# Kernel optimization log

Hardware: AMD Instinct MI355X
Metric: run time of the kernel (lower is better)

The kernel has to match this reference:

```python
import jax, jax.numpy as jnp
import numpy as np

NPRE = 8        # diffusion iterations (production default 8000; math identical per step)
DEPS = 0.1
LAMBDA = 0.24
K_PM = 0.03     # exp(log(0.03)) buffer in the 'none' branch
ALPHA = 0.7
SIGMA_FREQ = 0.1


def _g_pm(x, K):
    # Perona-Malik conductance g(x) = 1 / (1 + |x^2| / K^2)
    return 1.0 / (1.0 + jnp.abs(x * x) / (K * K))


def _gaussian_blur3(x, sigma):
    # Replicates torch create_gaussian_kernel(3, sigma): linspace(-3//2, 3//2, 3) = [-2, -0.5, 1]
    xs = jnp.linspace(-2.0, 1.0, 3)
    g1 = jnp.exp(-(xs ** 2) / (2.0 * sigma * sigma))
    g1 = g1 / g1.sum()
    k2 = jnp.outer(g1, g1).astype(x.dtype)            # [3,3]
    C = x.shape[1]
    k = jnp.broadcast_to(k2, (C, 1, 3, 3))
    xp = jnp.pad(x, ((0, 0), (0, 0), (1, 1), (1, 1)), mode='reflect')
    return jax.lax.conv_general_dilated(
        xp, k, window_strides=(1, 1), padding='VALID',
        dimension_numbers=('NCHW', 'OIHW', 'NCHW'), feature_group_count=C)


def _edge_coeffs(I, K):
    # c(I): FFT high-pass edge response + finite differences -> Perona-Malik coefficients
    b, c_, h, w = I.shape
    F = jnp.fft.fft2(I, norm='ortho')
    y = jnp.linspace(-1.0, 1.0, h)[:, None]
    xg = jnp.linspace(-1.0, 1.0, w)[None, :]
    hf_mask = (jnp.sqrt(xg * xg + y * y) > 0.5).astype(I.dtype)   # [h,w]
    er = jnp.real(jnp.fft.ifft2(F * hf_mask, norm='ortho'))
    dv = jnp.abs(I[:, :, 1:, :] - I[:, :, :-1, :]) + er[:, :, 1:, :]
    dh = jnp.abs(I[:, :, :, 1:] - I[:, :, :, :-1]) + er[:, :, :, 1:]
    cv = _g_pm(jnp.mean(dv, axis=1, keepdims=True), K)   # [b,1,h-1,w]
    ch = _g_pm(jnp.mean(dh, axis=1, keepdims=True), K)   # [b,1,h,w-1]
    return cv, ch


def _diffuse_step(cv, ch, I, l=LAMBDA):
    # frequency-domain smoothing branch
    Ff = jnp.fft.fft2(I, norm='ortho')
    sr = _gaussian_blur3(jnp.real(Ff), SIGMA_FREQ)
    si = _gaussian_blur3(jnp.imag(Ff), SIGMA_FREQ)
    I_freq = jnp.real(jnp.fft.ifft2(jax.lax.complex(sr, si), norm='ortho'))
    dv = I[:, :, 1:, :] - I[:, :, :-1, :]
    dh = I[:, :, :, 1:] - I[:, :, :, :-1]
    I = ALPHA * I + (1.0 - ALPHA) * I_freq
    tv = l * cv * dv
    th = l * ch * dh
    I = I.at[:, :, 1:, :].add(-tv).at[:, :, :-1, :].add(tv)
    I = I.at[:, :, :, 1:].add(-th).at[:, :, :, :-1].add(th)
    return I


def _adjust_step(img, source, mask_inv, eps=1e-8):
    b, c_, h, w = img.shape
    sh, sw = source.shape[2], source.shape[3]
    fh, fw = h // sh, w // sw
    # AdaptiveAvgPool2d((sh,sw)) with integer factor == block mean
    img_ss = img.reshape(b, c_, sh, fh, sw, fw).mean(axis=(3, 5))
    ratio_ss = jnp.where(mask_inv, jnp.ones_like(img_ss), source / (img_ss + eps))
    # nearest upsample with integer factor == repeat
    ratio = jnp.repeat(jnp.repeat(ratio_ss, fh, axis=2), fw, axis=3)
    return img * ratio


def setup_inputs() -> dict:
    key = jax.random.key(0)
    k1, k2, k3, k4 = jax.random.split(key, 4)
    guide = jax.random.normal(k1, (4, 3, 1024, 1024), dtype=jnp.float32)
    source = jax.random.uniform(k2, (4, 1, 128, 128), dtype=jnp.float32)
    mask_lr = jax.random.uniform(k3, (4, 1, 128, 128), dtype=jnp.float32)
    y_bicubic = jax.random.uniform(k4, (4, 1, 1024, 1024), dtype=jnp.float32)
    return {"guide": guide, "source": source, "mask_lr": mask_lr, "y_bicubic": y_bicubic}


def reference(guide, source, mask_lr, y_bicubic):
    # depth shift when source.min() <= deps (uniform[0,1) source -> effectively always)
    shift = jnp.where(jnp.min(source) <= DEPS, DEPS, 0.0).astype(source.dtype)
    source = source + shift
    img = y_bicubic + shift
    mask_inv = mask_lr < 0.5

    # 'none' feature extractor: guide_feats = cat([guide, img], 1) -> [B,4,H,W]
    feats = jnp.concatenate([guide, img], axis=1)
    cv, ch = _edge_coeffs(feats, K_PM)

    def step(I, _):
        I = _diffuse_step(cv, ch, I)
        I = _adjust_step(I, source, mask_inv)
        return I, None

    img, _ = jax.lax.scan(step, img, None, length=NPRE)
    return img - shift
```

## Files before the change

kernel.cpp:

```cpp
#include <hip/hip_runtime.h>
#include <hip/hip_fp16.h>

namespace {

constexpr int H = 1024, W = 1024, NB = 4;
constexpr int SH = 128, SW = 128;
constexpr float LAM = 0.24f;
constexpr float KK = 0.03f * 0.03f;
constexpr float DEPS_V = 0.1f;
constexpr float FFT_SCALE = 1.0f / (1024.0f * 1024.0f);
constexpr int COL_LO = 256, NCOL = 512;

__device__ __forceinline__ float2 cadd(float2 a, float2 b) { return make_float2(a.x + b.x, a.y + b.y); }
__device__ __forceinline__ float2 csub(float2 a, float2 b) { return make_float2(a.x - b.x, a.y - b.y); }
__device__ __forceinline__ float2 cmul(float2 a, float2 b) {
  return make_float2(a.x * b.x - a.y * b.y, a.x * b.y + a.y * b.x);
}
__device__ __forceinline__ int phys2(int e) { return e + (e >> 4); }

__global__ void k_shift_part(const float* __restrict__ src, float* __restrict__ partial) {
  int t = threadIdx.x;
  int b0 = blockIdx.x * 1024;
  float m = fminf(fminf(src[b0 + t], src[b0 + t + 256]),
                  fminf(src[b0 + t + 512], src[b0 + t + 768]));
  for (int o = 32; o > 0; o >>= 1) m = fminf(m, __shfl_xor(m, o));
  __shared__ float sm[4];
  if ((t & 63) == 0) sm[t >> 6] = m;
  __syncthreads();
  if (t == 0) partial[blockIdx.x] = fminf(fminf(sm[0], sm[1]), fminf(sm[2], sm[3]));
}

__global__ void k_shift_fin(const float* __restrict__ partial, float* __restrict__ shiftp) {
  int t = threadIdx.x;
  float m = partial[t];
  for (int o = 32; o > 0; o >>= 1) m = fminf(m, __shfl_xor(m, o));
  if (t == 0) shiftp[0] = (m <= DEPS_V) ? DEPS_V : 0.0f;
}

template <int NS, bool INV>
__device__ __forceinline__ void r4_butterfly(float2 v[4], int j, float2 r[4]) {
  if (NS > 1) {
    int p = j & (NS - 1);
    float sn, cs;
    sincospif((INV ? 1.0f : -1.0f) * (float)p * (1.0f / (float)(2 * NS)), &sn, &cs);
    float2 w1 = make_float2(cs, sn);
    float2 w2 = cmul(w1, w1);
    float2 w3 = cmul(w2, w1);
    v[1] = cmul(v[1], w1);
    v[2] = cmul(v[2], w2);
    v[3] = cmul(v[3], w3);
  }
  float2 a0 = cadd(v[0], v[2]), a2 = csub(v[0], v[2]);
  float2 a1 = cadd(v[1], v[3]), a3 = csub(v[1], v[3]);
  a3 = INV ? make_float2(-a3.y, a3.x) : make_float2(a3.y, -a3.x);
  r[0] = cadd(a0, a1);
  r[2] = csub(a0, a1);
  r[1] = cadd(a2, a3);
  r[3] = csub(a2, a3);
}

template <int NS, bool INV>
__device__ __forceinline__ void r4_stage_lds(float2 v[4], float2* dst, int j) {
  float2 r[4];
  r4_butterfly<NS, INV>(v, j, r);
  int p = j & (NS - 1);
  int base = ((j - p) << 2) + p;
#pragma unroll
  for (int k = 0; k < 4; ++k) dst[phys2(base + k * NS)] = r[k];
}

__device__ __forceinline__ void lds_load4(const float2* src, float2 v[4], int j) {
#pragma unroll
  for (int k = 0; k < 4; ++k) v[k] = src[phys2(j + k * 256)];
}

template <bool INV>
__device__ void fft1024(float2 v[4], float2* b0, float2* b1, int j) {
  r4_stage_lds<1, INV>(v, b0, j);
  __syncthreads();
  lds_load4(b0, v, j);
  r4_stage_lds<4, INV>(v, b1, j);
  __syncthreads();
  lds_load4(b1, v, j);
  r4_stage_lds<16, INV>(v, b0, j);
  __syncthreads();
  lds_load4(b0, v, j);
  r4_stage_lds<64, INV>(v, b1, j);
  __syncthreads();
  lds_load4(b1, v, j);
  float2 r[4];
  r4_butterfly<256, INV>(v, j, r);
#pragma unroll
  for (int k = 0; k < 4; ++k) v[k] = r[k];
}

__global__ void k_rowfft_fwd(const float* __restrict__ guide, const float* __restrict__ ybic,
                             const float* __restrict__ shiftp, float2* __restrict__ A) {
  __shared__ float2 b0[1088], b1[1088];
  int b = blockIdx.y, y0 = blockIdx.x * 2, j = threadIdx.x;
  float sh = shiftp[0];
  const float* g0 = guide + ((size_t)(b * 3 + 0) * H + y0) * W;
  const float* g1 = guide + ((size_t)(b * 3 + 1) * H + y0) * W;
  const float* g2 = guide + ((size_t)(b * 3 + 2) * H + y0) * W;
  const float* yb = ybic + ((size_t)b * H + y0) * W;
  float2 v[4];
#pragma unroll
  for (int k = 0; k < 4; ++k) {
    int x = j + k * 256;
    float s0 = g0[x] + g1[x] + g2[x] + (yb[x] + sh);
    float s1 = g0[x + W] + g1[x + W] + g2[x + W] + (yb[x + W] + sh);
    v[k] = make_float2(s0, s1);
  }
  fft1024<false>(v, b0, b1, j);
#pragma unroll
  for (int k = 0; k < 4; ++k) b0[phys2(j + k * 256)] = v[k];
  __syncthreads();
  float2* o0 = A + ((size_t)b * H + y0) * W;
  float2* o1 = o0 + W;
#pragma unroll
  for (int k = 0; k < 4; ++k) {
    int m = j + k * 256;
    float2 Zm = v[k];
    float2 Zc = b0[phys2((1024 - m) & 1023)];
    o0[m] = make_float2(0.5f * (Zm.x + Zc.x), 0.5f * (Zm.y - Zc.y));
    o1[m] = make_float2(0.5f * (Zm.y + Zc.y), 0.5f * (Zc.x - Zm.x));
  }
}

__global__ void k_transpose_fwd(const float2* __restrict__ A, float2* __restrict__ Bc) {
  __shared__ float2 tile[32][33];
  int b = blockIdx.z;
  int c0 = blockIdx.x * 32, y0 = blockIdx.y * 32;
  const float2* ip = A + (size_t)b * H * W;
  float2* op = Bc + (size_t)b * NCOL * H;
#pragma unroll
  for (int k = 0; k < 4; ++k)
    tile[threadIdx.y + k * 8][threadIdx.x] =
        ip[(size_t)(y0 + threadIdx.y + k * 8) * W + (COL_LO + c0 + threadIdx.x)];
  __syncthreads();
#pragma unroll
  for (int k = 0; k < 4; ++k)
    op[(size_t)(c0 + threadIdx.y + k * 8) * H + (y0 + threadIdx.x)] =
        tile[threadIdx.x][threadIdx.y + k * 8];
}

__global__ void k_colfft_mask(float2* __restrict__ Bc) {
  __shared__ float2 b0[1088], b1[1088];
  int b = blockIdx.y, r = blockIdx.x, j = threadIdx.x;
  int k2 = COL_LO + r;
  double xj = -1.0 + 2.0 * (double)k2 / 1023.0;
  double xj2 = xj * xj;
  float2* row = Bc + ((size_t)b * NCOL + r) * H;
  float2 v[4];
#pragma unroll
  for (int k = 0; k < 4; ++k) v[k] = row[j + k * 256];
  fft1024<false>(v, b0, b1, j);
#pragma unroll
  for (int k = 0; k < 4; ++k) {
    int i = j + k * 256;
    double yv = -1.0 + 2.0 * (double)i / 1023.0;
    if (xj2 + yv * yv <= 0.25) v[k] = make_float2(0.0f, 0.0f);
  }
  fft1024<true>(v, b0, b1, j);
#pragma unroll
  for (int k = 0; k < 4; ++k) row[j + k * 256] = v[k];
}

__global__ __launch_bounds__(256, 3) void k_invcoeffs(
    const float2* __restrict__ A, const float2* __restrict__ Bc,
    const float* __restrict__ guide, const float* __restrict__ ybic,
    __half2* __restrict__ cvh) {
  __shared__ float2 b0[1088], b1[1088];
  __shared__ float2 stage[5][NCOL];
  __shared__ float erbuf[2][1028];
  const int b = blockIdx.y, j = threadIdx.x;
  const int y0 = blockIdx.x * 4;
  const float2* Ab = A + (size_t)b * H * W;
  const float* g = guide + (size_t)b * 3 * H * W;
  const float* yb = ybic + (size_t)b * H * W;
  __half2* cpo = cvh + (size_t)b * H * W;
  const size_t CH = (size_t)H * W;

#pragma unroll
  for (int cc = 0; cc < 2; ++cc) {
    int c = j + cc * 256;
    const float2* bp = Bc + ((size_t)b * NCOL + c) * H + y0;
    float4 p01 = *(const float4*)bp;
    float4 p23 = *(const float4*)(bp + 2);
    float2 p4 = (y0 + 4 < H) ? bp[4] : make_float2(0.f, 0.f);
    stage[0][c] = make_float2(p01.x, p01.y);
    stage[1][c] = make_float2(p01.z, p01.w);
    stage[2][c] = make_float2(p23.x, p23.y);
    stage[3][c] = make_float2(p23.z, p23.w);
    stage[4][c] = p4;
  }
  __syncthreads();

  const int x0 = j * 4;
  for (int r = 0; r < 5; ++r) {
    int yf = y0 + r;
    if (yf < H) {
      const float2* arow = Ab + (size_t)yf * W;
      float2 v[4];
      float2 a0 = arow[j], a3 = arow[j + 768];
      v[0] = make_float2(a0.x * 1024.0f, a0.y * 1024.0f);
      v[3] = make_float2(a3.x * 1024.0f, a3.y * 1024.0f);
      v[1] = stage[r][j];
      v[2] = stage[r][j + 256];
      fft1024<true>(v, b0, b1, j);
#pragma unroll
      for (int k = 0; k < 4; ++k) erbuf[r & 1][j + k * 256] = v[k].x * FFT_SCALE;
    }
    __syncthreads();
    if (r >= 1) {
      int y = y0 + r - 1;
      size_t row = (size_t)y * W + x0;
      float4 a0 = *(const float4*)(g + row);
      float4 a1 = *(const float4*)(g + CH + row);
      float4 a2 = *(const float4*)(g + 2 * CH + row);
      float4 a3 = *(const float4*)(yb + row);
      float4 e0 = *(const float4*)&erbuf[(r - 1) & 1][x0];
      float A0[5] = {a0.x, a0.y, a0.z, a0.w, 0.f};
      float A1[5] = {a1.x, a1.y, a1.z, a1.w, 0.f};
      float A2[5] = {a2.x, a2.y, a2.z, a2.w, 0.f};
      float A3[5] = {a3.x, a3.y, a3.z, a3.w, 0.f};
      float E0[5] = {e0.x, e0.y, e0.z, e0.w, 0.f};
      bool hasR = (x0 + 4 < W);
      if (hasR) {
        A0[4] = g[row + 4]; A1[4] = g[CH + row + 4]; A2[4] = g[2 * CH + row + 4];
        A3[4] = yb[row + 4]; E0[4] = erbuf[(r - 1) & 1][x0 + 4];
      }
      float B0[4], B1[4], B2[4], B3[4], E1[4];
      bool hasD = (y < H - 1);
      if (hasD) {
        float4 q0 = *(const float4*)(g + row + W);
        float4 q1 = *(const float4*)(g + CH + row + W);
        float4 q2 = *(const float4*)(g + 2 * CH + row + W);
        float4 q3 = *(const float4*)(yb + row + W);
        float4 q4 = *(const float4*)&erbuf[r & 1][x0];
        B0[0]=q0.x; B0[1]=q0.y; B0[2]=q0.z; B0[3]=q0.w;
        B1[0]=q1.x; B1[1]=q1.y; B1[2]=q1.z; B1[3]=q1.w;
        B2[0]=q2.x; B2[1]=q2.y; B2[2]=q2.z; B2[3]=q2.w;
        B3[0]=q3.x; B3[1]=q3.y; B3[2]=q3.z; B3[3]=q3.w;
        E1[0]=q4.x; E1[1]=q4.y; E1[2]=q4.z; E1[3]=q4.w;
      }
      __half2 outq[4];
#pragma unroll
      for (int i = 0; i < 4; ++i) {
        float cvv = 0.0f;
        if (hasD) {
          float s = fabsf(B0[i] - A0[i]) + fabsf(B1[i] - A1[i]) +
                    fabsf(B2[i] - A2[i]) + fabsf(B3[i] - A3[i]);
          s = (s + E1[i]) * 0.25f;
          cvv = 1.0f / (1.0f + (s * s) / KK);
        }
        float chv = 0.0f;
        if (i < 3 || hasR) {
          float s = fabsf(A0[i + 1] - A0[i]) + fabsf(A1[i + 1] - A1[i]) +
                    fabsf(A2[i + 1] - A2[i]) + fabsf(A3[i + 1] - A3[i]);
          s = (s + E0[i + 1]) * 0.25f;
          chv = 1.0f / (1.0f + (s * s) / KK);
        }
        outq[i] = __floats2half2_rn(cvv, chv);
      }
      *(float4*)(cpo + row) = *(const float4*)outq;
    }
    __syncthreads();
  }
}

template <bool FIRST, bool FINAL>
__global__ void k_diffuse_ratio(const float* __restrict__ in, const float* __restrict__ ratio_in,
                                const float* __restrict__ shiftp,
                                const __half2* __restrict__ cvh, const float* __restrict__ src,
                                const float* __restrict__ mask, float* __restrict__ out,
                                float* __restrict__ ratio_out) {
  int b = blockIdx.z, tx = threadIdx.x, ty = threadIdx.y;
  int x0 = blockIdx.x * 128 + tx * 4;
  int y = blockIdx.y * 8 + ty;
  float sh = shiftp[0];
  float addv = FIRST ? sh : 0.0f;
  size_t base = (size_t)b * H * W;
  const float* I = in + base;
  const __half2* cp = cvh + base;
  float rq = 1.f, rup = 1.f, rdn = 1.f, rlf = 1.f, rrt = 1.f;
  if (!FIRST) {
    const float* rb = ratio_in + (size_t)b * SH * SW;
    int bx3 = x0 >> 3, byq = y >> 3;
    rq = rb[byq * SW + bx3];
    rup = (y > 0) ? rb[((y - 1) >> 3) * SW + bx3] : 1.f;
    rdn = (y < H - 1) ? rb[((y + 1) >> 3) * SW + bx3] : 1.f;
    rlf = (x0 > 0) ? rb[byq * SW + ((x0 - 1) >> 3)] : 1.f;
    rrt = (x0 + 4 < W) ? rb[byq * SW + ((x0 + 4) >> 3)] : 1.f;
  }
  size_t row = (size_t)y * W + x0;
  bool hasU = (y > 0), hasD = (y < H - 1);
  float4 c4 = *(const float4*)(I + row);
  float C[4] = {(c4.x + addv) * rq, (c4.y + addv) * rq, (c4.z + addv) * rq, (c4.w + addv) * rq};
  float U[4] = {0, 0, 0, 0}, D[4] = {0, 0, 0, 0};
  if (hasU) {
    float4 u4 = *(const float4*)(I + row - W);
    U[0] = (u4.x + addv) * rup; U[1] = (u4.y + addv) * rup;
    U[2] = (u4.z + addv) * rup; U[3] = (u4.w + addv) * rup;
  }
  if (hasD) {
    float4 d4 = *(const float4*)(I + row + W);
    D[0] = (d4.x + addv) * rdn; D[1] = (d4.y + addv) * rdn;
    D[2] = (d4.z + addv) * rdn; D[3] = (d4.w + addv) * rdn;
  }
  float lf = (x0 > 0) ? (I[row - 1] + addv) * rlf : 0.f;
  float rt = (x0 + 4 < W) ? (I[row + 4] + addv) * rrt : 0.f;
  float4 ccraw = *(const float4*)(cp + row);
  const __half2* hq = (const __half2*)&ccraw;
  float cvq[4], chq[4];
#pragma unroll
  for (int i = 0; i < 4; ++i) {
    float2 tt = __half22float2(hq[i]);
    cvq[i] = tt.x; chq[i] = tt.y;
  }
  float cvu[4] = {0, 0, 0, 0};
  if (hasU) {
    float4 cu = *(const float4*)(cp + row - W);
    const __half2* hu = (const __half2*)&cu;
#pragma unroll
    for (int i = 0; i < 4; ++i) cvu[i] = __half2float(hu[i].x);
  }
  float chl = (x0 > 0) ? __half2float(cp[row - 1].y) : 0.f;
  float acc[4];
#pragma unroll
  for (int i = 0; i < 4; ++i) {
    float L = (i == 0) ? lf : C[i - 1];
    float R = (i == 3) ? rt : C[i + 1];
    float cL = (i == 0) ? chl : chq[i - 1];
    float a = C[i];
    if (hasD) a += LAM * cvq[i] * (D[i] - C[i]);
    if (hasU) a -= LAM * cvu[i] * (C[i] - U[i]);
    if (i < 3 || x0 + 4 < W) a += LAM * chq[i] * (R - C[i]);
    if (i > 0 || x0 > 0) a -= LAM * cL * (C[i] - L);
    acc[i] = a;
  }
  __shared__ float sd[8][32];
  __shared__ float rblk[16];
  sd[ty][tx] = acc[0] + acc[1] + acc[2] + acc[3];
  __syncthreads();
  if (ty == 0) {
    float colsum = 0.f;
#pragma unroll
    for (int r = 0; r < 8; ++r) colsum += sd[r][tx];
    float s = colsum + __shfl_down(colsum, 1);
    if ((tx & 1) == 0) {
      int pb = tx >> 1;
      size_t si = ((size_t)b * SH + blockIdx.y) * SW + (blockIdx.x * 16 + pb);
      float mean = s * (1.0f / 64.0f);
      float rv = (mask[si] < 0.5f) ? 1.0f : (src[si] + sh) / (mean + 1e-8f);
      if (FINAL) rblk[pb] = rv;
      else ratio_out[si] = rv;
    }
  }
  if (FINAL) {
    __syncthreads();
    float rv = rblk[tx >> 1];
    float4 o = make_float4(acc[0] * rv - sh, acc[1] * rv - sh, acc[2] * rv - sh, acc[3] * rv - sh);
    *(float4*)(out + base + row) = o;
  } else {
    *(float4*)(out + base + row) = make_float4(acc[0], acc[1], acc[2], acc[3]);
  }
}

}

extern "C" void kernel_launch(void* const* d_in, const int* in_sizes, int n_in, void* d_out,
                              int out_size, void* d_ws, size_t ws_size, hipStream_t stream) {
  (void)in_sizes; (void)n_in; (void)out_size; (void)ws_size;
  const float* guide = (const float*)d_in[0];
  const float* source = (const float*)d_in[1];
  const float* mask = (const float*)d_in[2];
  const float* ybic = (const float*)d_in[3];
  float* out = (float*)d_out;

  char* ws = (char*)d_ws;
  float2* A = (float2*)ws;
  float2* Bc = (float2*)(ws + (size_t)32 * 1024 * 1024);
  __half2* cvh = (__half2*)(ws + (size_t)48 * 1024 * 1024);
  float* itmp = (float*)ws;
  float* shiftp = (float*)(ws + (size_t)64 * 1024 * 1024);
  float* partial = shiftp + 64;
  float* ratioA = (float*)(ws + (size_t)64 * 1024 * 1024 + 4096);
  float* ratioB = ratioA + (size_t)NB * SH * SW;

  k_shift_part<<<64, 256, 0, stream>>>(source, partial);
  k_shift_fin<<<1, 64, 0, stream>>>(partial, shiftp);

  k_rowfft_fwd<<<dim3(H / 2, NB), 256, 0, stream>>>(guide, ybic, shiftp, A);
  dim3 gT(NCOL / 32, H / 32, NB), bT(32, 8);
  k_transpose_fwd<<<gT, bT, 0, stream>>>(A, Bc);
  k_colfft_mask<<<dim3(NCOL, NB), 256, 0, stream>>>(Bc);
  k_invcoeffs<<<dim3(H / 4, NB), 256, 0, stream>>>(A, Bc, guide, ybic, cvh);

  dim3 gD(W / 128, H / 8, NB), bD(32, 8);
  k_diffuse_ratio<true, false><<<gD, bD, 0, stream>>>(ybic, nullptr, shiftp, cvh, source, mask,
                                                      itmp, ratioA);
  k_diffuse_ratio<false, false><<<gD, bD, 0, stream>>>(itmp, ratioA, shiftp, cvh, source, mask,
                                                       out, ratioB);
  k_diffuse_ratio<false, false><<<gD, bD, 0, stream>>>(out, ratioB, shiftp, cvh, source, mask,
                                                       itmp, ratioA);
  k_diffuse_ratio<false, false><<<gD, bD, 0, stream>>>(itmp, ratioA, shiftp, cvh, source, mask,
                                                       out, ratioB);
  k_diffuse_ratio<false, false><<<gD, bD, 0, stream>>>(out, ratioB, shiftp, cvh, source, mask,
                                                       itmp, ratioA);
  k_diffuse_ratio<false, false><<<gD, bD, 0, stream>>>(itmp, ratioA, shiftp, cvh, source, mask,
                                                       out, ratioB);
  k_diffuse_ratio<false, false><<<gD, bD, 0, stream>>>(out, ratioB, shiftp, cvh, source, mask,
                                                       itmp, ratioA);
  k_diffuse_ratio<false, true><<<gD, bD, 0, stream>>>(itmp, ratioA, shiftp, cvh, source, mask,
                                                      out, ratioB);
}
```

Baseline: 290.2 us.

## Process eight rows per block in inverse-FFT coefficient kernel with two concurrent FFTs

The inverse row-FFT plus coefficient kernel now handles eight output rows per block with 512 threads. Two half-blocks each run an independent 1024-point FFT at the same time, which cuts the redundant halo-row FFT from one per four rows to one per eight rows and halves the number of sync phases per row. The staged shared-memory load of column data is replaced by direct strided global reads. The diffusion ping-pong now uses two scratch buffers and writes the output only on the final step, which avoids using the output as an intermediate buffer. Risks include uncoalesced strided loads of the column data and higher shared-memory and register pressure per block.

```diff
diff --git a/kernel.cpp b/kernel.cpp
--- a/kernel.cpp
+++ b/kernel.cpp
@@ -166,78 +166,74 @@
   for (int k = 0; k < 4; ++k) row[j + k * 256] = v[k];
 }
 
-__global__ __launch_bounds__(256, 3) void k_invcoeffs(
+__global__ __launch_bounds__(512, 4) void k_invcoeffs8(
     const float2* __restrict__ A, const float2* __restrict__ Bc,
     const float* __restrict__ guide, const float* __restrict__ ybic,
     __half2* __restrict__ cvh) {
-  __shared__ float2 b0[1088], b1[1088];
-  __shared__ float2 stage[5][NCOL];
-  __shared__ float erbuf[2][1028];
-  const int b = blockIdx.y, j = threadIdx.x;
-  const int y0 = blockIdx.x * 4;
+  __shared__ float2 fb0[2][1088], fb1[2][1088];
+  __shared__ float erbuf[4][1028];
+  const int b = blockIdx.y;
+  const int y0 = blockIdx.x * 8;
+  const int tid = threadIdx.x;
+  const int j = tid & 255;
+  const int half = tid >> 8;
+  float2* b0 = fb0[half];
+  float2* b1 = fb1[half];
   const float2* Ab = A + (size_t)b * H * W;
   const float* g = guide + (size_t)b * 3 * H * W;
   const float* yb = ybic + (size_t)b * H * W;
   __half2* cpo = cvh + (size_t)b * H * W;
   const size_t CH = (size_t)H * W;
-
-#pragma unroll
-  for (int cc = 0; cc < 2; ++cc) {
-    int c = j + cc * 256;
-    const float2* bp = Bc + ((size_t)b * NCOL + c) * H + y0;
-    float4 p01 = *(const float4*)bp;
-    float4 p23 = *(const float4*)(bp + 2);
-    float2 p4 = (y0 + 4 < H) ? bp[4] : make_float2(0.f, 0.f);
-    stage[0][c] = make_float2(p01.x, p01.y);
-    stage[1][c] = make_float2(p01.z, p01.w);
-    stage[2][c] = make_float2(p23.x, p23.y);
-    stage[3][c] = make_float2(p23.z, p23.w);
-    stage[4][c] = p4;
-  }
-  __syncthreads();
-
   const int x0 = j * 4;
-  for (int r = 0; r < 5; ++r) {
-    int yf = y0 + r;
-    if (yf < H) {
-      const float2* arow = Ab + (size_t)yf * W;
+  const bool hasR = (x0 + 4 < W);
+
+  for (int p = 0; p <= 4; ++p) {
+    int er_idx = 2 * p + half;
+    int row = y0 + er_idx;
+    bool valid = (er_idx <= 8) && (row < H);
+    int rowc = valid ? row : (H - 1);
+    {
+      const float2* arow = Ab + (size_t)rowc * W;
       float2 v[4];
       float2 a0 = arow[j], a3 = arow[j + 768];
       v[0] = make_float2(a0.x * 1024.0f, a0.y * 1024.0f);
       v[3] = make_float2(a3.x * 1024.0f, a3.y * 1024.0f);
-      v[1] = stage[r][j];
-      v[2] = stage[r][j + 256];
+      v[1] = Bc[((size_t)b * NCOL + j) * H + rowc];
+      v[2] = Bc[((size_t)b * NCOL + j + 256) * H + rowc];
       fft1024<true>(v, b0, b1, j);
-#pragma unroll
-      for (int k = 0; k < 4; ++k) erbuf[r & 1][j + k * 256] = v[k].x * FFT_SCALE;
+      if (valid) {
+#pragma unroll
+        for (int k = 0; k < 4; ++k) erbuf[er_idx & 3][j + k * 256] = v[k].x * FFT_SCALE;
+      }
     }
     __syncthreads();
-    if (r >= 1) {
-      int y = y0 + r - 1;
-      size_t row = (size_t)y * W + x0;
-      float4 a0 = *(const float4*)(g + row);
-      float4 a1 = *(const float4*)(g + CH + row);
-      float4 a2 = *(const float4*)(g + 2 * CH + row);
-      float4 a3 = *(const float4*)(yb + row);
-      float4 e0 = *(const float4*)&erbuf[(r - 1) & 1][x0];
+    if (p >= 1) {
+      int rel = 2 * (p - 1) + half;
+      int y = y0 + rel;
+      int s0i = rel & 3, s1i = (rel + 1) & 3;
+      size_t row4 = (size_t)y * W + x0;
+      float4 a0 = *(const float4*)(g + row4);
+      float4 a1 = *(const float4*)(g + CH + row4);
+      float4 a2 = *(const float4*)(g + 2 * CH + row4);
+      float4 a3 = *(const float4*)(yb + row4);
+      float4 e0 = *(const float4*)&erbuf[s0i][x0];
       float A0[5] = {a0.x, a0.y, a0.z, a0.w, 0.f};
       float A1[5] = {a1.x, a1.y, a1.z, a1.w, 0.f};
       float A2[5] = {a2.x, a2.y, a2.z, a2.w, 0.f};
       float A3[5] = {a3.x, a3.y, a3.z, a3.w, 0.f};
       float E0[5] = {e0.x, e0.y, e0.z, e0.w, 0.f};
-      bool hasR = (x0 + 4 < W);
       if (hasR) {
-        A0[4] = g[row + 4]; A1[4] = g[CH + row + 4]; A2[4] = g[2 * CH + row + 4];
-        A3[4] = yb[row + 4]; E0[4] = erbuf[(r - 1) & 1][x0 + 4];
+        A0[4] = g[row4 + 4]; A1[4] = g[CH + row4 + 4]; A2[4] = g[2 * CH + row4 + 4];
+        A3[4] = yb[row4 + 4]; E0[4] = erbuf[s0i][x0 + 4];
       }
       float B0[4], B1[4], B2[4], B3[4], E1[4];
       bool hasD = (y < H - 1);
       if (hasD) {
-        float4 q0 = *(const float4*)(g + row + W);
-        float4 q1 = *(const float4*)(g + CH + row + W);
-        float4 q2 = *(const float4*)(g + 2 * CH + row + W);
-        float4 q3 = *(const float4*)(yb + row + W);
-        float4 q4 = *(const float4*)&erbuf[r & 1][x0];
+        float4 q0 = *(const float4*)(g + row4 + W);
+        float4 q1 = *(const float4*)(g + CH + row4 + W);
+        float4 q2 = *(const float4*)(g + 2 * CH + row4 + W);
+        float4 q3 = *(const float4*)(yb + row4 + W);
+        float4 q4 = *(const float4*)&erbuf[s1i][x0];
         B0[0]=q0.x; B0[1]=q0.y; B0[2]=q0.z; B0[3]=q0.w;
         B1[0]=q1.x; B1[1]=q1.y; B1[2]=q1.z; B1[3]=q1.w;
         B2[0]=q2.x; B2[1]=q2.y; B2[2]=q2.z; B2[3]=q2.w;
@@ -263,7 +259,7 @@
         }
         outq[i] = __floats2half2_rn(cvv, chv);
       }
-      *(float4*)(cpo + row) = *(const float4*)outq;
+      *(float4*)(cpo + row4) = *(const float4*)outq;
     }
     __syncthreads();
   }
@@ -382,7 +378,8 @@
   float2* A = (float2*)ws;
   float2* Bc = (float2*)(ws + (size_t)32 * 1024 * 1024);
   __half2* cvh = (__half2*)(ws + (size_t)48 * 1024 * 1024);
-  float* itmp = (float*)ws;
+  float* bufA = (float*)ws;
+  float* bufB = (float*)(ws + (size_t)16 * 1024 * 1024);
   float* shiftp = (float*)(ws + (size_t)64 * 1024 * 1024);
   float* partial = shiftp + 64;
   float* ratioA = (float*)(ws + (size_t)64 * 1024 * 1024 + 4096);
@@ -395,23 +392,23 @@
   dim3 gT(NCOL / 32, H / 32, NB), bT(32, 8);
   k_transpose_fwd<<<gT, bT, 0, stream>>>(A, Bc);
   k_colfft_mask<<<dim3(NCOL, NB), 256, 0, stream>>>(Bc);
-  k_invcoeffs<<<dim3(H / 4, NB), 256, 0, stream>>>(A, Bc, guide, ybic, cvh);
+  k_invcoeffs8<<<dim3(H / 8, NB), 512, 0, stream>>>(A, Bc, guide, ybic, cvh);
 
   dim3 gD(W / 128, H / 8, NB), bD(32, 8);
   k_diffuse_ratio<true, false><<<gD, bD, 0, stream>>>(ybic, nullptr, shiftp, cvh, source, mask,
-                                                      itmp, ratioA);
-  k_diffuse_ratio<false, false><<<gD, bD, 0, stream>>>(itmp, ratioA, shiftp, cvh, source, mask,
-                                                       out, ratioB);
-  k_diffuse_ratio<false, false><<<gD, bD, 0, stream>>>(out, ratioB, shiftp, cvh, source, mask,
-                                                       itmp, ratioA);
-  k_diffuse_ratio<false, false><<<gD, bD, 0, stream>>>(itmp, ratioA, shiftp, cvh, source, mask,
-                                                       out, ratioB);
-  k_diffuse_ratio<false, false><<<gD, bD, 0, stream>>>(out, ratioB, shiftp, cvh, source, mask,
-                                                       itmp, ratioA);
-  k_diffuse_ratio<false, false><<<gD, bD, 0, stream>>>(itmp, ratioA, shiftp, cvh, source, mask,
-                                                       out, ratioB);
-  k_diffuse_ratio<false, false><<<gD, bD, 0, stream>>>(out, ratioB, shiftp, cvh, source, mask,
-                                                       itmp, ratioA);
-  k_diffuse_ratio<false, true><<<gD, bD, 0, stream>>>(itmp, ratioA, shiftp, cvh, source, mask,
+                                                      bufA, ratioA);
+  k_diffuse_ratio<false, false><<<gD, bD, 0, stream>>>(bufA, ratioA, shiftp, cvh, source, mask,
+                                                       bufB, ratioB);
+  k_diffuse_ratio<false, false><<<gD, bD, 0, stream>>>(bufB, ratioB, shiftp, cvh, source, mask,
+                                                       bufA, ratioA);
+  k_diffuse_ratio<false, false><<<gD, bD, 0, stream>>>(bufA, ratioA, shiftp, cvh, source, mask,
+                                                       bufB, ratioB);
+  k_diffuse_ratio<false, false><<<gD, bD, 0, stream>>>(bufB, ratioB, shiftp, cvh, source, mask,
+                                                       bufA, ratioA);
+  k_diffuse_ratio<false, false><<<gD, bD, 0, stream>>>(bufA, ratioA, shiftp, cvh, source, mask,
+                                                       bufB, ratioB);
+  k_diffuse_ratio<false, false><<<gD, bD, 0, stream>>>(bufB, ratioB, shiftp, cvh, source, mask,
+                                                       bufA, ratioA);
+  k_diffuse_ratio<false, true><<<gD, bD, 0, stream>>>(bufA, ratioA, shiftp, cvh, source, mask,
                                                       out, ratioB);
 }
```

After: 304.4 us. 4.9% more time.
